# Performance work log

Measured on AMD Instinct MI355X. Metric: run time of the kernel, lower is better.

The kernel has to match this reference:

```python
import jax, jax.numpy as jnp
import numpy as np

N = 163842   # icosahedron level-7 vertices
CH = 64
EPS = 1e-5
SLOPE = 0.2

def _bn_lrelu(x, g, b):
    # BatchNorm1d over vertex dim (training-mode batch stats, biased var) + LeakyReLU(0.2)
    mu = jnp.mean(x, axis=0)
    var = jnp.var(x, axis=0)
    y = (x - mu) * jax.lax.rsqrt(var + EPS) * g + b
    return jnp.where(y > 0, y, SLOPE * y)

def _onering_conv(x, neigh, W, bias):
    # gather 7 one-ring neighbors per vertex, flatten, linear project
    n = x.shape[0]
    feat = x[neigh].reshape(n, -1)          # [N, 7*C]
    return feat @ W + bias                  # [N, out]

def setup_inputs() -> dict:
    key = jax.random.key(0)
    ks = jax.random.split(key, 8)
    d = {
        "x": jax.random.normal(ks[0], (N, CH), jnp.float32),
        "neigh_orders": jax.random.randint(ks[1], (7 * N,), 0, N, jnp.int64),
    }
    for i, k in enumerate([1, 2, 3, 4]):
        cin = CH * k
        d[f"g{k}"] = jnp.ones((cin,), jnp.float32)
        d[f"b{k}"] = jnp.zeros((cin,), jnp.float32)
        d[f"W{k}"] = jax.random.normal(ks[2 + i], (7 * cin, CH), jnp.float32) * (1.0 / np.sqrt(7 * cin))
        d[f"wb{k}"] = jnp.zeros((CH,), jnp.float32)
    return d

def reference(x, neigh_orders, g1, b1, g2, b2, g3, b3, g4, b4,
              W1, wb1, W2, wb2, W3, wb3, W4, wb4):
    x1 = _onering_conv(_bn_lrelu(x, g1, b1), neigh_orders, W1, wb1)
    c2 = jnp.concatenate((x, x1), axis=1)
    x2 = _onering_conv(_bn_lrelu(c2, g2, b2), neigh_orders, W2, wb2)
    c3 = jnp.concatenate((x, x1, x2), axis=1)
    x3 = _onering_conv(_bn_lrelu(c3, g3, b3), neigh_orders, W3, wb3)
    c4 = jnp.concatenate((x, x1, x2, x3), axis=1)
    x4 = _onering_conv(_bn_lrelu(c4, g4, b4), neigh_orders, W4, wb4)
    return x4
```

## Files before the change

### kernel.cpp

```cpp
#include <hip/hip_runtime.h>
#include <stdint.h>

#define NV 163842
#define PARTS 512
#define EPSV 1e-5f

using short8 = __attribute__((ext_vector_type(8))) short;
using f32x4  = __attribute__((ext_vector_type(4))) float;

static __device__ __forceinline__ float bf2f(unsigned short u) {
    union { unsigned int i; float f; } v; v.i = ((unsigned int)u) << 16; return v.f;
}
static __device__ __forceinline__ unsigned short f2bf(float f) {
    union { float f; unsigned int i; } v; v.f = f;
    return (unsigned short)((v.i + 0x7FFFu + ((v.i >> 16) & 1u)) >> 16);
}
static __device__ __forceinline__ void bf2x(unsigned int w, float& a, float& b) {
    union { unsigned int i; float f; } lo, hi;
    lo.i = w << 16; hi.i = w & 0xFFFF0000u;
    a = lo.f; b = hi.f;
}

__global__ __launch_bounds__(256) void k_cast(const float* __restrict__ x,
                                              unsigned short* __restrict__ C) {
    int e = blockIdx.x * 256 + threadIdx.x;
    if (e >= NV * 16) return;
    int v = e >> 4;
    int c = (e & 15) << 2;
    float4 f = *(const float4*)(x + (size_t)v * 64 + c);
    ushort4 u;
    u.x = f2bf(f.x); u.y = f2bf(f.y); u.z = f2bf(f.z); u.w = f2bf(f.w);
    *(ushort4*)(C + (size_t)v * 256 + c) = u;
}

template<int CIN>
__global__ __launch_bounds__(256) void k_reduce(const unsigned short* __restrict__ C,
                                                float* __restrict__ part) {
    constexpr int TPR = CIN / 8;
    constexpr int RPB = 256 / TPR;
    constexpr int ACTIVE = TPR * RPB;
    int t = threadIdx.x, b = blockIdx.x;
    int c8 = t % TPR, ro = t / TPR;
    float s[8], s2[8];
#pragma unroll
    for (int j = 0; j < 8; ++j) { s[j] = 0.f; s2[j] = 0.f; }
    if (t < ACTIVE) {
        for (int row = b * RPB + ro; row < NV; row += PARTS * RPB) {
            uint4 u = *(const uint4*)(C + (size_t)row * 256 + c8 * 8);
            float f[8];
            bf2x(u.x, f[0], f[1]); bf2x(u.y, f[2], f[3]);
            bf2x(u.z, f[4], f[5]); bf2x(u.w, f[6], f[7]);
#pragma unroll
            for (int j = 0; j < 8; ++j) { s[j] += f[j]; s2[j] += f[j] * f[j]; }
        }
    }
    __shared__ float red[2048];
#pragma unroll
    for (int j = 0; j < 8; ++j) red[t * 8 + j] = s[j];
    __syncthreads();
    if (t < TPR) {
        float a[8];
#pragma unroll
        for (int j = 0; j < 8; ++j) a[j] = red[t * 8 + j];
        for (int r2 = 1; r2 < RPB; ++r2)
#pragma unroll
            for (int j = 0; j < 8; ++j) a[j] += red[(r2 * TPR + t) * 8 + j];
#pragma unroll
        for (int j = 0; j < 8; ++j) part[(size_t)b * 512 + t * 8 + j] = a[j];
    }
    __syncthreads();
#pragma unroll
    for (int j = 0; j < 8; ++j) red[t * 8 + j] = s2[j];
    __syncthreads();
    if (t < TPR) {
        float a[8];
#pragma unroll
        for (int j = 0; j < 8; ++j) a[j] = red[t * 8 + j];
        for (int r2 = 1; r2 < RPB; ++r2)
#pragma unroll
            for (int j = 0; j < 8; ++j) a[j] += red[(r2 * TPR + t) * 8 + j];
#pragma unroll
        for (int j = 0; j < 8; ++j) part[(size_t)b * 512 + 256 + t * 8 + j] = a[j];
    }
}

__global__ __launch_bounds__(256) void k_finalize(const float* __restrict__ part,
                                                  const float* __restrict__ g,
                                                  const float* __restrict__ bb,
                                                  float* __restrict__ ss, int cin) {
    int t = threadIdx.x;
    if (t >= cin) return;
    float s = 0.f, s2 = 0.f;
    for (int p = 0; p < PARTS; ++p) {
        s  += part[(size_t)p * 512 + t];
        s2 += part[(size_t)p * 512 + 256 + t];
    }
    float mu  = s * (1.0f / NV);
    float var = s2 * (1.0f / NV) - mu * mu;
    float sc  = g[t] * rsqrtf(var + EPSV);
    ss[t] = sc;
    ss[256 + t] = bb[t] - mu * sc;
}

template<int CIN>
__global__ __launch_bounds__(256) void k_apply(const unsigned short* __restrict__ C,
                                               const float* __restrict__ ss,
                                               unsigned short* __restrict__ Y) {
    __shared__ float ssc[256], ssh[256];
    int t = threadIdx.x;
    ssc[t] = ss[t]; ssh[t] = ss[256 + t];
    __syncthreads();
    int e = blockIdx.x * 256 + t;
    constexpr int TOT8 = (int)((long long)NV * CIN / 8);
    if (e >= TOT8) return;
    int base = e * 8;
    int v = base / CIN;
    int c = base - v * CIN;
    uint4 u = *(const uint4*)(C + (size_t)v * 256 + c);
    float f[8];
    bf2x(u.x, f[0], f[1]); bf2x(u.y, f[2], f[3]);
    bf2x(u.z, f[4], f[5]); bf2x(u.w, f[6], f[7]);
    unsigned int ob[8];
#pragma unroll
    for (int j = 0; j < 8; ++j) {
        float yv = f[j] * ssc[c + j] + ssh[c + j];
        yv = yv > 0.f ? yv : 0.2f * yv;
        ob[j] = f2bf(yv);
    }
    uint4 o;
    o.x = ob[0] | (ob[1] << 16); o.y = ob[2] | (ob[3] << 16);
    o.z = ob[4] | (ob[5] << 16); o.w = ob[6] | (ob[7] << 16);
    *(uint4*)(Y + (size_t)v * CIN + c) = o;
}

__global__ __launch_bounds__(256) void k_wt(const float* __restrict__ W,
                                            unsigned short* __restrict__ Wt, int K7) {
    int j = blockIdx.x * 256 + threadIdx.x;
    if (j >= 64 * K7) return;
    int n = j / K7, k = j - n * K7;
    Wt[j] = f2bf(W[(size_t)k * 64 + n]);
}

template<int CIN, bool FINAL>
__global__ __launch_bounds__(256) void k_gg(const unsigned short* __restrict__ Y,
                                            const int* __restrict__ neigh,
                                            const unsigned short* __restrict__ Wt,
                                            const float* __restrict__ wb,
                                            unsigned short* __restrict__ Cout,
                                            float* __restrict__ Fout) {
    constexpr int K7 = 7 * CIN;
    __shared__ int sIdx[448];
    __shared__ unsigned short sA[64 * 72];
    __shared__ unsigned short sW[64 * 72];
    const int t = threadIdx.x;
    const int v0 = blockIdx.x * 64;

    for (int q = t; q < 448; q += 256) {
        int gi = v0 * 7 + q;
        sIdx[q] = (gi < NV * 7) ? neigh[gi] : 0;
    }
    __syncthreads();

    const int wv = t >> 6, lane = t & 63;
    const int m = lane & 15, quad = lane >> 4;
    const int row = t >> 2, q4 = t & 3;

    f32x4 acc[4];
#pragma unroll
    for (int i = 0; i < 4; ++i) acc[i] = f32x4{0.f, 0.f, 0.f, 0.f};

    const int aRd = (wv * 16 + m) * 72 + quad * 8;

    for (int r = 0; r < 7; ++r) {
        const int kidx = sIdx[row * 7 + r];
        const unsigned short* ybase = Y + (size_t)kidx * CIN;
#pragma unroll
        for (int kb = 0; kb < CIN; kb += 64) {
            const uint4* srcA = (const uint4*)(ybase + kb + q4 * 16);
            uint4 a0 = srcA[0], a1 = srcA[1];
            const uint4* srcW = (const uint4*)(Wt + (size_t)row * K7 + r * CIN + kb + q4 * 16);
            uint4 w0 = srcW[0], w1 = srcW[1];
            *(uint4*)(sA + row * 72 + q4 * 16)     = a0;
            *(uint4*)(sA + row * 72 + q4 * 16 + 8) = a1;
            *(uint4*)(sW + row * 72 + q4 * 16)     = w0;
            *(uint4*)(sW + row * 72 + q4 * 16 + 8) = w1;
            __syncthreads();
#pragma unroll
            for (int s = 0; s < 2; ++s) {
                short8 af = *(const short8*)(sA + aRd + s * 32);
#pragma unroll
                for (int ct = 0; ct < 4; ++ct) {
                    short8 bf = *(const short8*)(sW + (ct * 16 + m) * 72 + s * 32 + quad * 8);
                    acc[ct] = __builtin_amdgcn_mfma_f32_16x16x32_bf16(af, bf, acc[ct], 0, 0, 0);
                }
            }
            __syncthreads();
        }
    }
#pragma unroll
    for (int ct = 0; ct < 4; ++ct) {
        int col = ct * 16 + m;
        float bv = wb[col];
#pragma unroll
        for (int j = 0; j < 4; ++j) {
            int vr = v0 + wv * 16 + quad * 4 + j;
            if (vr < NV) {
                float val = acc[ct][j] + bv;
                if (FINAL) Fout[(size_t)vr * 64 + col] = val;
                else       Cout[(size_t)vr * 256 + col] = f2bf(val);
            }
        }
    }
}

template<int CIN, bool FINAL>
static void run_layer(const unsigned short* C, unsigned short* Yb, unsigned short* WT,
                      float* PART, float* SS, const int* neigh,
                      const float* g, const float* bb, const float* W, const float* wb,
                      unsigned short* Cout, float* Fout, hipStream_t stream) {
    k_reduce<CIN><<<PARTS, 256, 0, stream>>>(C, PART);
    k_finalize<<<1, 256, 0, stream>>>(PART, g, bb, SS, CIN);
    constexpr int TOT8 = (int)((long long)NV * CIN / 8);
    k_apply<CIN><<<(TOT8 + 255) / 256, 256, 0, stream>>>(C, SS, Yb);
    const int K7 = 7 * CIN;
    k_wt<<<(64 * K7 + 255) / 256, 256, 0, stream>>>(W, WT, K7);
    k_gg<CIN, FINAL><<<(NV + 63) / 64, 256, 0, stream>>>(Yb, neigh, WT, wb, Cout, Fout);
}

extern "C" void kernel_launch(void* const* d_in, const int* in_sizes, int n_in,
                              void* d_out, int out_size, void* d_ws, size_t ws_size,
                              hipStream_t stream) {
    const float* x     = (const float*)d_in[0];
    const int*   neigh = (const int*)d_in[1];
    const float* G[4]  = {(const float*)d_in[2],  (const float*)d_in[6],
                          (const float*)d_in[10], (const float*)d_in[14]};
    const float* B[4]  = {(const float*)d_in[3],  (const float*)d_in[7],
                          (const float*)d_in[11], (const float*)d_in[15]};
    const float* W[4]  = {(const float*)d_in[4],  (const float*)d_in[8],
                          (const float*)d_in[12], (const float*)d_in[16]};
    const float* WB[4] = {(const float*)d_in[5],  (const float*)d_in[9],
                          (const float*)d_in[13], (const float*)d_in[17]};
    float* out = (float*)d_out;

    char* ws = (char*)d_ws;
    size_t off = 0;
    unsigned short* C  = (unsigned short*)(ws + off); off += (size_t)NV * 256 * 2;
    unsigned short* Yb = (unsigned short*)(ws + off); off += (size_t)NV * 256 * 2;
    unsigned short* WT = (unsigned short*)(ws + off); off += (size_t)64 * 1792 * 2;
    float* PART        = (float*)(ws + off);          off += (size_t)PARTS * 512 * 4;
    float* SS          = (float*)(ws + off);          off += 512 * 4;

    k_cast<<<(NV * 16 + 255) / 256, 256, 0, stream>>>(x, C);
    run_layer< 64, false>(C, Yb, WT, PART, SS, neigh, G[0], B[0], W[0], WB[0], C +  64, nullptr, stream);
    run_layer<128, false>(C, Yb, WT, PART, SS, neigh, G[1], B[1], W[1], WB[1], C + 128, nullptr, stream);
    run_layer<192, false>(C, Yb, WT, PART, SS, neigh, G[2], B[2], W[2], WB[2], C + 192, nullptr, stream);
    run_layer<256, true >(C, Yb, WT, PART, SS, neigh, G[3], B[3], W[3], WB[3], nullptr, out,     stream);
}
```

Baseline: 593.3 us.

## Fuse BN stats into producer epilogues and BN-apply into gather GEMM

Per-channel sum and sum-of-squares are now accumulated with atomics in the cast kernel and in each conv epilogue, so the separate reduce and finalize passes go away. The BN scale/shift and LeakyReLU are applied while the gathered rows are staged into shared memory, which removes the apply kernel and the Yb intermediate buffer. The GEMM tile grows to 128 vertices with a register prefetch of the next chunk, and all four weight transposes are done in one launch. The trade-offs are float atomics (non-deterministic summation order), recomputing the normalization on every gathered neighbor, and a single-pass variance formula.

```diff
diff --git a/kernel.cpp b/kernel.cpp
--- a/kernel.cpp
+++ b/kernel.cpp
@@ -2,15 +2,11 @@
 #include <stdint.h>
 
 #define NV 163842
-#define PARTS 512
 #define EPSV 1e-5f
 
 using short8 = __attribute__((ext_vector_type(8))) short;
 using f32x4  = __attribute__((ext_vector_type(4))) float;
 
-static __device__ __forceinline__ float bf2f(unsigned short u) {
-    union { unsigned int i; float f; } v; v.i = ((unsigned int)u) << 16; return v.f;
-}
 static __device__ __forceinline__ unsigned short f2bf(float f) {
     union { float f; unsigned int i; } v; v.f = f;
     return (unsigned short)((v.i + 0x7FFFu + ((v.i >> 16) & 1u)) >> 16);
@@ -20,142 +16,118 @@
     lo.i = w << 16; hi.i = w & 0xFFFF0000u;
     a = lo.f; b = hi.f;
 }
+static __device__ __forceinline__ unsigned int pack2(float a, float b) {
+    union { float f; unsigned int i; } ua, ub; ua.f = a; ub.f = b;
+    return __builtin_amdgcn_perm(ub.i + 0x8000u, ua.i + 0x8000u, 0x07060302);
+}
+
+__global__ __launch_bounds__(256) void k_zero(float* __restrict__ ACC) {
+    ACC[threadIdx.x] = 0.f;
+    ACC[256 + threadIdx.x] = 0.f;
+}
 
 __global__ __launch_bounds__(256) void k_cast(const float* __restrict__ x,
-                                              unsigned short* __restrict__ C) {
-    int e = blockIdx.x * 256 + threadIdx.x;
-    if (e >= NV * 16) return;
-    int v = e >> 4;
-    int c = (e & 15) << 2;
-    float4 f = *(const float4*)(x + (size_t)v * 64 + c);
-    ushort4 u;
-    u.x = f2bf(f.x); u.y = f2bf(f.y); u.z = f2bf(f.z); u.w = f2bf(f.w);
-    *(ushort4*)(C + (size_t)v * 256 + c) = u;
-}
-
-template<int CIN>
-__global__ __launch_bounds__(256) void k_reduce(const unsigned short* __restrict__ C,
-                                                float* __restrict__ part) {
-    constexpr int TPR = CIN / 8;
-    constexpr int RPB = 256 / TPR;
-    constexpr int ACTIVE = TPR * RPB;
-    int t = threadIdx.x, b = blockIdx.x;
-    int c8 = t % TPR, ro = t / TPR;
-    float s[8], s2[8];
-#pragma unroll
-    for (int j = 0; j < 8; ++j) { s[j] = 0.f; s2[j] = 0.f; }
-    if (t < ACTIVE) {
-        for (int row = b * RPB + ro; row < NV; row += PARTS * RPB) {
-            uint4 u = *(const uint4*)(C + (size_t)row * 256 + c8 * 8);
-            float f[8];
-            bf2x(u.x, f[0], f[1]); bf2x(u.y, f[2], f[3]);
-            bf2x(u.z, f[4], f[5]); bf2x(u.w, f[6], f[7]);
-#pragma unroll
-            for (int j = 0; j < 8; ++j) { s[j] += f[j]; s2[j] += f[j] * f[j]; }
-        }
-    }
-    __shared__ float red[2048];
-#pragma unroll
-    for (int j = 0; j < 8; ++j) red[t * 8 + j] = s[j];
+                                              unsigned short* __restrict__ C,
+                                              float* __restrict__ ACC) {
+    const int t = threadIdx.x;
+    const int wv = t >> 6, lane = t & 63;
+    const int v = blockIdx.x * 64 + (t >> 2);
+    const int c0 = (t & 3) * 16;
+    float f[16];
+    const bool valid = v < NV;
+    if (valid) {
+        const float4* p = (const float4*)(x + (size_t)v * 64 + c0);
+#pragma unroll
+        for (int i = 0; i < 4; ++i) {
+            float4 q = p[i];
+            f[i * 4 + 0] = q.x; f[i * 4 + 1] = q.y; f[i * 4 + 2] = q.z; f[i * 4 + 3] = q.w;
+        }
+        unsigned int o[8];
+#pragma unroll
+        for (int i = 0; i < 8; ++i)
+            o[i] = ((unsigned int)f2bf(f[2 * i])) | (((unsigned int)f2bf(f[2 * i + 1])) << 16);
+        uint4* dst = (uint4*)(C + (size_t)v * 256 + c0);
+        dst[0] = uint4{o[0], o[1], o[2], o[3]};
+        dst[1] = uint4{o[4], o[5], o[6], o[7]};
+    } else {
+#pragma unroll
+        for (int i = 0; i < 16; ++i) f[i] = 0.f;
+    }
+    float s[16], s2[16];
+#pragma unroll
+    for (int i = 0; i < 16; ++i) { s[i] = f[i]; s2[i] = f[i] * f[i]; }
+#pragma unroll
+    for (int mask = 4; mask <= 32; mask <<= 1) {
+#pragma unroll
+        for (int i = 0; i < 16; ++i) {
+            s[i]  += __shfl_xor(s[i],  mask);
+            s2[i] += __shfl_xor(s2[i], mask);
+        }
+    }
+    __shared__ float red[4 * 128];
+    if ((lane >> 2) == 0) {
+        int cb = (lane & 3) * 16;
+#pragma unroll
+        for (int i = 0; i < 16; ++i) {
+            red[wv * 128 + cb + i]      = s[i];
+            red[wv * 128 + 64 + cb + i] = s2[i];
+        }
+    }
     __syncthreads();
-    if (t < TPR) {
-        float a[8];
-#pragma unroll
-        for (int j = 0; j < 8; ++j) a[j] = red[t * 8 + j];
-        for (int r2 = 1; r2 < RPB; ++r2)
-#pragma unroll
-            for (int j = 0; j < 8; ++j) a[j] += red[(r2 * TPR + t) * 8 + j];
-#pragma unroll
-        for (int j = 0; j < 8; ++j) part[(size_t)b * 512 + t * 8 + j] = a[j];
-    }
-    __syncthreads();
-#pragma unroll
-    for (int j = 0; j < 8; ++j) red[t * 8 + j] = s2[j];
-    __syncthreads();
-    if (t < TPR) {
-        float a[8];
-#pragma unroll
-        for (int j = 0; j < 8; ++j) a[j] = red[t * 8 + j];
-        for (int r2 = 1; r2 < RPB; ++r2)
-#pragma unroll
-            for (int j = 0; j < 8; ++j) a[j] += red[(r2 * TPR + t) * 8 + j];
-#pragma unroll
-        for (int j = 0; j < 8; ++j) part[(size_t)b * 512 + 256 + t * 8 + j] = a[j];
-    }
-}
-
-__global__ __launch_bounds__(256) void k_finalize(const float* __restrict__ part,
-                                                  const float* __restrict__ g,
-                                                  const float* __restrict__ bb,
-                                                  float* __restrict__ ss, int cin) {
-    int t = threadIdx.x;
-    if (t >= cin) return;
-    float s = 0.f, s2 = 0.f;
-    for (int p = 0; p < PARTS; ++p) {
-        s  += part[(size_t)p * 512 + t];
-        s2 += part[(size_t)p * 512 + 256 + t];
-    }
-    float mu  = s * (1.0f / NV);
-    float var = s2 * (1.0f / NV) - mu * mu;
-    float sc  = g[t] * rsqrtf(var + EPSV);
-    ss[t] = sc;
-    ss[256 + t] = bb[t] - mu * sc;
-}
-
-template<int CIN>
-__global__ __launch_bounds__(256) void k_apply(const unsigned short* __restrict__ C,
-                                               const float* __restrict__ ss,
-                                               unsigned short* __restrict__ Y) {
-    __shared__ float ssc[256], ssh[256];
-    int t = threadIdx.x;
-    ssc[t] = ss[t]; ssh[t] = ss[256 + t];
-    __syncthreads();
-    int e = blockIdx.x * 256 + t;
-    constexpr int TOT8 = (int)((long long)NV * CIN / 8);
-    if (e >= TOT8) return;
-    int base = e * 8;
-    int v = base / CIN;
-    int c = base - v * CIN;
-    uint4 u = *(const uint4*)(C + (size_t)v * 256 + c);
-    float f[8];
-    bf2x(u.x, f[0], f[1]); bf2x(u.y, f[2], f[3]);
-    bf2x(u.z, f[4], f[5]); bf2x(u.w, f[6], f[7]);
-    unsigned int ob[8];
-#pragma unroll
-    for (int j = 0; j < 8; ++j) {
-        float yv = f[j] * ssc[c + j] + ssh[c + j];
-        yv = yv > 0.f ? yv : 0.2f * yv;
-        ob[j] = f2bf(yv);
-    }
-    uint4 o;
-    o.x = ob[0] | (ob[1] << 16); o.y = ob[2] | (ob[3] << 16);
-    o.z = ob[4] | (ob[5] << 16); o.w = ob[6] | (ob[7] << 16);
-    *(uint4*)(Y + (size_t)v * CIN + c) = o;
-}
-
-__global__ __launch_bounds__(256) void k_wt(const float* __restrict__ W,
-                                            unsigned short* __restrict__ Wt, int K7) {
+    if (t < 128) {
+        float v4 = red[t] + red[128 + t] + red[256 + t] + red[384 + t];
+        int c = t & 63, which = t >> 6;
+        atomicAdd(&ACC[which * 256 + c], v4);
+    }
+}
+
+__global__ __launch_bounds__(256) void k_wt_all(const float* __restrict__ W1,
+                                                const float* __restrict__ W2,
+                                                const float* __restrict__ W3,
+                                                const float* __restrict__ W4,
+                                                unsigned short* __restrict__ WT) {
     int j = blockIdx.x * 256 + threadIdx.x;
-    if (j >= 64 * K7) return;
-    int n = j / K7, k = j - n * K7;
-    Wt[j] = f2bf(W[(size_t)k * 64 + n]);
-}
-
-template<int CIN, bool FINAL>
-__global__ __launch_bounds__(256) void k_gg(const unsigned short* __restrict__ Y,
+    if (j >= 286720) return;
+    const float* W; int jj, K7;
+    if (j < 28672)       { W = W1; jj = j;          K7 = 448;  }
+    else if (j < 86016)  { W = W2; jj = j - 28672;  K7 = 896;  }
+    else if (j < 172032) { W = W3; jj = j - 86016;  K7 = 1344; }
+    else                 { W = W4; jj = j - 172032; K7 = 1792; }
+    int n = jj / K7, k = jj - n * K7;
+    WT[j] = f2bf(W[(size_t)k * 64 + n]);
+}
+
+template<int CIN, int GRP, bool FINAL>
+__global__ __launch_bounds__(256) void k_gg(const unsigned short* __restrict__ C,
                                             const int* __restrict__ neigh,
-                                            const unsigned short* __restrict__ Wt,
+                                            const unsigned short* __restrict__ WT,
+                                            const float* __restrict__ g,
+                                            const float* __restrict__ bglob,
                                             const float* __restrict__ wb,
+                                            float* __restrict__ ACC,
                                             unsigned short* __restrict__ Cout,
                                             float* __restrict__ Fout) {
+    constexpr int KB = CIN / 64;
+    constexpr int NC = 7 * KB;
     constexpr int K7 = 7 * CIN;
-    __shared__ int sIdx[448];
-    __shared__ unsigned short sA[64 * 72];
+
+    __shared__ float ssc[256], ssh[256];
+    __shared__ int sIdx[896];
+    __shared__ unsigned short sA[128 * 72];
     __shared__ unsigned short sW[64 * 72];
+
     const int t = threadIdx.x;
-    const int v0 = blockIdx.x * 64;
-
-    for (int q = t; q < 448; q += 256) {
+    const int v0 = blockIdx.x * 128;
+
+    if (t < CIN) {
+        float s = ACC[t], s2 = ACC[256 + t];
+        float mu = s * (1.0f / NV);
+        float var = fmaf(-mu, mu, s2 * (1.0f / NV));
+        float sc = g[t] * rsqrtf(var + EPSV);
+        ssc[t] = sc;
+        ssh[t] = bglob[t] - mu * sc;
+    }
+    for (int q = t; q < 896; q += 256) {
         int gi = v0 * 7 + q;
         sIdx[q] = (gi < NV * 7) ? neigh[gi] : 0;
     }
@@ -163,68 +135,121 @@
 
     const int wv = t >> 6, lane = t & 63;
     const int m = lane & 15, quad = lane >> 4;
-    const int row = t >> 2, q4 = t & 3;
-
-    f32x4 acc[4];
-#pragma unroll
-    for (int i = 0; i < 4; ++i) acc[i] = f32x4{0.f, 0.f, 0.f, 0.f};
-
-    const int aRd = (wv * 16 + m) * 72 + quad * 8;
-
-    for (int r = 0; r < 7; ++r) {
-        const int kidx = sIdx[row * 7 + r];
-        const unsigned short* ybase = Y + (size_t)kidx * CIN;
-#pragma unroll
-        for (int kb = 0; kb < CIN; kb += 64) {
-            const uint4* srcA = (const uint4*)(ybase + kb + q4 * 16);
-            uint4 a0 = srcA[0], a1 = srcA[1];
-            const uint4* srcW = (const uint4*)(Wt + (size_t)row * K7 + r * CIN + kb + q4 * 16);
-            uint4 w0 = srcW[0], w1 = srcW[1];
-            *(uint4*)(sA + row * 72 + q4 * 16)     = a0;
-            *(uint4*)(sA + row * 72 + q4 * 16 + 8) = a1;
-            *(uint4*)(sW + row * 72 + q4 * 16)     = w0;
-            *(uint4*)(sW + row * 72 + q4 * 16 + 8) = w1;
-            __syncthreads();
-#pragma unroll
-            for (int s = 0; s < 2; ++s) {
-                short8 af = *(const short8*)(sA + aRd + s * 32);
-#pragma unroll
-                for (int ct = 0; ct < 4; ++ct) {
-                    short8 bf = *(const short8*)(sW + (ct * 16 + m) * 72 + s * 32 + quad * 8);
-                    acc[ct] = __builtin_amdgcn_mfma_f32_16x16x32_bf16(af, bf, acc[ct], 0, 0, 0);
+    const int arow = t >> 1, ahalf = t & 1;
+    const int wrow = t >> 2, wq = t & 3;
+
+    f32x4 acc[2][4];
+#pragma unroll
+    for (int i = 0; i < 2; ++i)
+#pragma unroll
+        for (int j = 0; j < 4; ++j) acc[i][j] = f32x4{0.f, 0.f, 0.f, 0.f};
+
+    auto load_chunk = [&](int c, uint4* aa, uint4& x0, uint4& x1) {
+        int r = c / KB, kb = c - r * KB;
+        int src = sIdx[arow * 7 + r];
+        const uint4* pa = (const uint4*)(C + (size_t)src * 256 + kb * 64 + ahalf * 32);
+        aa[0] = pa[0]; aa[1] = pa[1]; aa[2] = pa[2]; aa[3] = pa[3];
+        const uint4* pw = (const uint4*)(WT + (size_t)wrow * K7 + c * 64 + wq * 16);
+        x0 = pw[0]; x1 = pw[1];
+    };
+    auto stage = [&](const uint4* aa, uint4 x0, uint4 x1, int c) {
+        int kb = c - (c / KB) * KB;
+        int chb = kb * 64 + ahalf * 32;
+        unsigned short* dstA = sA + arow * 72 + ahalf * 32;
+#pragma unroll
+        for (int i = 0; i < 4; ++i) {
+            unsigned int u[4] = {aa[i].x, aa[i].y, aa[i].z, aa[i].w};
+            unsigned int o[4];
+#pragma unroll
+            for (int jj = 0; jj < 4; ++jj) {
+                float lo, hi; bf2x(u[jj], lo, hi);
+                int ch = chb + i * 8 + jj * 2;
+                float y0 = fmaf(lo, ssc[ch],     ssh[ch]);
+                float y1 = fmaf(hi, ssc[ch + 1], ssh[ch + 1]);
+                y0 = y0 > 0.f ? y0 : 0.2f * y0;
+                y1 = y1 > 0.f ? y1 : 0.2f * y1;
+                o[jj] = pack2(y0, y1);
+            }
+            *(uint4*)(dstA + i * 8) = uint4{o[0], o[1], o[2], o[3]};
+        }
+        *(uint4*)(sW + wrow * 72 + wq * 16)     = x0;
+        *(uint4*)(sW + wrow * 72 + wq * 16 + 8) = x1;
+    };
+
+    uint4 a[4], w0, w1;
+    load_chunk(0, a, w0, w1);
+#pragma unroll 2
+    for (int c = 0; c < NC; ++c) {
+        uint4 na[4], nw0, nw1;
+        if (c + 1 < NC) load_chunk(c + 1, na, nw0, nw1);
+        stage(a, w0, w1, c);
+        __syncthreads();
+#pragma unroll
+        for (int s = 0; s < 2; ++s) {
+            short8 af0 = *(const short8*)(sA + (wv * 32 + m) * 72      + s * 32 + quad * 8);
+            short8 af1 = *(const short8*)(sA + (wv * 32 + 16 + m) * 72 + s * 32 + quad * 8);
+#pragma unroll
+            for (int ct = 0; ct < 4; ++ct) {
+                short8 bf = *(const short8*)(sW + (ct * 16 + m) * 72 + s * 32 + quad * 8);
+                acc[0][ct] = __builtin_amdgcn_mfma_f32_16x16x32_bf16(af0, bf, acc[0][ct], 0, 0, 0);
+                acc[1][ct] = __builtin_amdgcn_mfma_f32_16x16x32_bf16(af1, bf, acc[1][ct], 0, 0, 0);
+            }
+        }
+        __syncthreads();
+        if (c + 1 < NC) {
+#pragma unroll
+            for (int i = 0; i < 4; ++i) a[i] = na[i];
+            w0 = nw0; w1 = nw1;
+        }
+    }
+
+    float bsum[4]  = {0.f, 0.f, 0.f, 0.f};
+    float b2sum[4] = {0.f, 0.f, 0.f, 0.f};
+#pragma unroll
+    for (int mt = 0; mt < 2; ++mt) {
+#pragma unroll
+        for (int ct = 0; ct < 4; ++ct) {
+            int col = ct * 16 + m;
+            float bv = wb[col];
+#pragma unroll
+            for (int j = 0; j < 4; ++j) {
+                int vr = v0 + wv * 32 + mt * 16 + quad * 4 + j;
+                float val = acc[mt][ct][j] + bv;
+                if (vr < NV) {
+                    if (FINAL) {
+                        Fout[(size_t)vr * 64 + col] = val;
+                    } else {
+                        Cout[(size_t)vr * 256 + GRP * 64 + col] = f2bf(val);
+                        bsum[ct] += val; b2sum[ct] += val * val;
+                    }
                 }
             }
-            __syncthreads();
-        }
-    }
-#pragma unroll
-    for (int ct = 0; ct < 4; ++ct) {
-        int col = ct * 16 + m;
-        float bv = wb[col];
-#pragma unroll
-        for (int j = 0; j < 4; ++j) {
-            int vr = v0 + wv * 16 + quad * 4 + j;
-            if (vr < NV) {
-                float val = acc[ct][j] + bv;
-                if (FINAL) Fout[(size_t)vr * 64 + col] = val;
-                else       Cout[(size_t)vr * 256 + col] = f2bf(val);
-            }
-        }
-    }
-}
-
-template<int CIN, bool FINAL>
-static void run_layer(const unsigned short* C, unsigned short* Yb, unsigned short* WT,
-                      float* PART, float* SS, const int* neigh,
-                      const float* g, const float* bb, const float* W, const float* wb,
-                      unsigned short* Cout, float* Fout, hipStream_t stream) {
-    k_reduce<CIN><<<PARTS, 256, 0, stream>>>(C, PART);
-    k_finalize<<<1, 256, 0, stream>>>(PART, g, bb, SS, CIN);
-    constexpr int TOT8 = (int)((long long)NV * CIN / 8);
-    k_apply<CIN><<<(TOT8 + 255) / 256, 256, 0, stream>>>(C, SS, Yb);
-    const int K7 = 7 * CIN;
-    k_wt<<<(64 * K7 + 255) / 256, 256, 0, stream>>>(W, WT, K7);
-    k_gg<CIN, FINAL><<<(NV + 63) / 64, 256, 0, stream>>>(Yb, neigh, WT, wb, Cout, Fout);
+        }
+    }
+    if (!FINAL) {
+#pragma unroll
+        for (int ct = 0; ct < 4; ++ct) {
+            bsum[ct]  += __shfl_xor(bsum[ct], 16);
+            bsum[ct]  += __shfl_xor(bsum[ct], 32);
+            b2sum[ct] += __shfl_xor(b2sum[ct], 16);
+            b2sum[ct] += __shfl_xor(b2sum[ct], 32);
+        }
+        float* red = (float*)sA;
+        if (quad == 0) {
+#pragma unroll
+            for (int ct = 0; ct < 4; ++ct) {
+                red[wv * 128 + ct * 16 + m]       = bsum[ct];
+                red[512 + wv * 128 + ct * 16 + m] = b2sum[ct];
+            }
+        }
+        __syncthreads();
+        if (t < 128) {
+            int c = t & 63, which = t >> 6;
+            float v = red[which * 512 + c] + red[which * 512 + 128 + c] +
+                      red[which * 512 + 256 + c] + red[which * 512 + 384 + c];
+            atomicAdd(&ACC[which * 256 + GRP * 64 + c], v);
+        }
+    }
 }
 
 extern "C" void kernel_launch(void* const* d_in, const int* in_sizes, int n_in,
@@ -245,14 +270,16 @@
     char* ws = (char*)d_ws;
     size_t off = 0;
     unsigned short* C  = (unsigned short*)(ws + off); off += (size_t)NV * 256 * 2;
-    unsigned short* Yb = (unsigned short*)(ws + off); off += (size_t)NV * 256 * 2;
-    unsigned short* WT = (unsigned short*)(ws + off); off += (size_t)64 * 1792 * 2;
-    float* PART        = (float*)(ws + off);          off += (size_t)PARTS * 512 * 4;
-    float* SS          = (float*)(ws + off);          off += 512 * 4;
-
-    k_cast<<<(NV * 16 + 255) / 256, 256, 0, stream>>>(x, C);
-    run_layer< 64, false>(C, Yb, WT, PART, SS, neigh, G[0], B[0], W[0], WB[0], C +  64, nullptr, stream);
-    run_layer<128, false>(C, Yb, WT, PART, SS, neigh, G[1], B[1], W[1], WB[1], C + 128, nullptr, stream);
-    run_layer<192, false>(C, Yb, WT, PART, SS, neigh, G[2], B[2], W[2], WB[2], C + 192, nullptr, stream);
-    run_layer<256, true >(C, Yb, WT, PART, SS, neigh, G[3], B[3], W[3], WB[3], nullptr, out,     stream);
-}
+    unsigned short* WT = (unsigned short*)(ws + off); off += (size_t)286720 * 2;
+    float* ACC         = (float*)(ws + off);          off += 512 * 4;
+
+    k_zero<<<1, 256, 0, stream>>>(ACC);
+    k_cast<<<(NV + 63) / 64, 256, 0, stream>>>(x, C, ACC);
+    k_wt_all<<<(286720 + 255) / 256, 256, 0, stream>>>(W[0], W[1], W[2], W[3], WT);
+
+    const int GG = (NV + 127) / 128;
+    k_gg< 64, 1, false><<<GG, 256, 0, stream>>>(C, neigh, WT,          G[0], B[0], WB[0], ACC, C, nullptr);
+    k_gg<128, 2, false><<<GG, 256, 0, stream>>>(C, neigh, WT + 28672,  G[1], B[1], WB[1], ACC, C, nullptr);
+    k_gg<192, 3, false><<<GG, 256, 0, stream>>>(C, neigh, WT + 86016,  G[2], B[2], WB[2], ACC, C, nullptr);
+    k_gg<256, 0, true ><<<GG, 256, 0, stream>>>(C, neigh, WT + 172032, G[3], B[3], WB[3], ACC, nullptr, out);
+}
```

Result: faster. 528.0 us (-11.0%).
